# Kernel optimization log

Measured on AMD Instinct MI355X. Metric: run time of the kernel, lower is better.

The kernel has to match this reference:

```python
import jax, jax.numpy as jnp
import numpy as np

B, T, C, H = 4, 2048, 512, 8
HS = C // H  # head_size = 64
EPS = 1e-5


def layernorm(x, g, b):
    mu = jnp.mean(x, axis=-1, keepdims=True)
    var = jnp.mean(jnp.square(x - mu), axis=-1, keepdims=True)
    return (x - mu) * jax.lax.rsqrt(var + EPS) * g + b


def setup_inputs() -> dict:
    key = jax.random.key(0)
    ks = jax.random.split(key, 12)
    s_attn = 1.0 / np.sqrt(C)
    s_ff1 = 1.0 / np.sqrt(C)
    s_ff2 = 1.0 / np.sqrt(4 * C)
    return {
        "x": jax.random.normal(ks[0], (B, T, C), jnp.float32),
        "wq": jax.random.normal(ks[1], (H, C, HS), jnp.float32) * s_attn,
        "wk": jax.random.normal(ks[2], (H, C, HS), jnp.float32) * s_attn,
        "wv": jax.random.normal(ks[3], (H, C, HS), jnp.float32) * s_attn,
        "w1": jax.random.normal(ks[4], (C, 4 * C), jnp.float32) * s_ff1,
        "b1": jnp.zeros((4 * C,), jnp.float32),
        "w2": jax.random.normal(ks[5], (4 * C, C), jnp.float32) * s_ff2,
        "b2": jnp.zeros((C,), jnp.float32),
        "ln1_g": jnp.ones((C,), jnp.float32),
        "ln1_b": jnp.zeros((C,), jnp.float32),
        "ln2_g": jnp.ones((C,), jnp.float32),
        "ln2_b": jnp.zeros((C,), jnp.float32),
    }


def reference(x, wq, wk, wv, w1, b1, w2, b2, ln1_g, ln1_b, ln2_g, ln2_b):
    # pre-LN multi-head causal self-attention
    h = layernorm(x, ln1_g, ln1_b)                       # [B,T,C]
    q = jnp.einsum("btc,hcd->bhtd", h, wq)
    k = jnp.einsum("btc,hcd->bhtd", h, wk)
    v = jnp.einsum("btc,hcd->bhtd", h, wv)
    # NOTE: source scales by full embed dim C, not head_size
    scores = jnp.einsum("bhtd,bhsd->bhts", q, k) * (C ** -0.5)  # [B,H,T,T]
    causal = jnp.tril(jnp.ones((T, T), bool))
    scores = jnp.where(causal, scores, -jnp.inf)
    att = jax.nn.softmax(scores, axis=-1)
    out = jnp.einsum("bhts,bhsd->bhtd", att, v)          # [B,H,T,HS]
    out = out.transpose(0, 2, 1, 3).reshape(B, T, C)     # concat heads
    x = x + out
    # FFN with residual
    h2 = layernorm(x, ln2_g, ln2_b)
    ff = jax.nn.relu(h2 @ w1 + b1) @ w2 + b2
    return x + ff
```

## Files before the change

### kernel.cpp

```cpp
#include <hip/hip_runtime.h>

typedef unsigned short ushort_t;
typedef __attribute__((ext_vector_type(8))) short short8;
typedef __attribute__((ext_vector_type(4))) float floatx4;

#define B_  4
#define T_  2048
#define C_  512
#define H_  8
#define HS_ 64
#define M_  (B_*T_)
#define SCALE2 0.06376140168547404f

__device__ __forceinline__ float b2f(ushort_t u) {
  union { unsigned int i; float f; } w; w.i = ((unsigned int)u) << 16; return w.f;
}
__device__ __forceinline__ ushort_t f2b(float f) {
  union { float f; unsigned int i; } w; w.f = f;
  unsigned int x = w.i;
  return (ushort_t)((x + 0x7fffu + ((x >> 16) & 1u)) >> 16);
}
__device__ __forceinline__ ushort_t f2b_fast(float f) {
  union { float f; unsigned int i; } w; w.f = f;
  return (ushort_t)((w.i + 0x8000u) >> 16);
}
__device__ __forceinline__ void gl_lds16(const ushort_t* g, ushort_t* l) {
  __builtin_amdgcn_global_load_lds((const unsigned int*)g, (unsigned int*)l, 16, 0, 0);
}

__global__ __launch_bounds__(256) void transpose_all(const float* __restrict__ wq,
                                                     const float* __restrict__ wk,
                                                     const float* __restrict__ wv,
                                                     const float* __restrict__ w1,
                                                     const float* __restrict__ w2,
                                                     ushort_t* __restrict__ qkvt,
                                                     ushort_t* __restrict__ w1t,
                                                     ushort_t* __restrict__ w2t) {
  __shared__ ushort_t t[32][33];
  int idx = blockIdx.x;
  const float* in; ushort_t* out; int K, N, bx, by, z = 0;
  if (idx < 768) {
    int seg = idx >> 8, li = idx & 255;
    in = seg == 0 ? wq : (seg == 1 ? wk : wv);
    out = qkvt + (size_t)seg * 262144;
    K = 512; N = 64;
    z = li >> 5; li &= 31;
    bx = li & 1; by = li >> 1;
  } else if (idx < 1792) {
    int li = idx - 768;
    in = w1; out = w1t; K = 512; N = 2048;
    bx = li & 63; by = li >> 6;
  } else {
    int li = idx - 1792;
    in = w2; out = w2t; K = 2048; N = 512;
    bx = li & 15; by = li >> 4;
  }
  size_t zoff = (size_t)z * K * N;
  int n0 = bx * 32, k0 = by * 32;
  int tx = threadIdx.x & 31, ty = threadIdx.x >> 5;
#pragma unroll
  for (int i = 0; i < 4; i++)
    t[ty + 8 * i][tx] = f2b(in[zoff + (size_t)(k0 + ty + 8 * i) * N + n0 + tx]);
  __syncthreads();
#pragma unroll
  for (int i = 0; i < 4; i++)
    out[zoff + (size_t)(n0 + ty + 8 * i) * K + k0 + tx] = t[tx][ty + 8 * i];
}

__global__ __launch_bounds__(256) void ln_k(const float* __restrict__ X,
                                            const float* __restrict__ g,
                                            const float* __restrict__ bb,
                                            ushort_t* __restrict__ Y) {
  int wave = threadIdx.x >> 6, lane = threadIdx.x & 63;
  size_t row = (size_t)blockIdx.x * 4 + wave;
  float v[8], s = 0.f, s2 = 0.f;
#pragma unroll
  for (int i = 0; i < 8; i++) {
    float x = X[row * C_ + lane + 64 * i];
    v[i] = x; s += x; s2 += x * x;
  }
#pragma unroll
  for (int off = 32; off >= 1; off >>= 1) {
    s += __shfl_xor(s, off); s2 += __shfl_xor(s2, off);
  }
  float mu = s * (1.0f / C_);
  float var = s2 * (1.0f / C_) - mu * mu;
  float rs = rsqrtf(var + 1e-5f);
  ushort_t* yr = Y + row * C_;
#pragma unroll
  for (int i = 0; i < 8; i++) {
    int c = lane + 64 * i;
    yr[c] = f2b((v[i] - mu) * rs * g[c] + bb[c]);
  }
}

__global__ __launch_bounds__(256) void gemm_bt128(const ushort_t* __restrict__ A,
                                                  const ushort_t* __restrict__ Bt,
                                                  ushort_t* __restrict__ Out,
                                                  int K, int ldOut,
                                                  const float* __restrict__ bias,
                                                  int relu) {
  __shared__ __align__(16) ushort_t As[128 * 64];
  __shared__ __align__(16) ushort_t Bs[128 * 64];
  const int tid = threadIdx.x;
  const int lane = tid & 63, wave = tid >> 6;
  const long row0 = (long)blockIdx.x * 128;
  const long col0 = (long)blockIdx.y * 128;
  const int srow = wave * 32 + (lane >> 3);
  const int scol = (((lane & 7) ^ ((lane >> 3) & 7))) * 8;
  const ushort_t* Ab = A + (size_t)(row0 + srow) * K + scol;
  const ushort_t* Bb = Bt + (size_t)(col0 + srow) * K + scol;
  const int wm = (wave >> 1) * 64, wn = (wave & 1) * 64;
  const int fq = lane >> 4, fl = lane & 15;
  floatx4 acc[4][4] = {};

  for (int k0 = 0; k0 < K; k0 += 64) {
    __syncthreads();
#pragma unroll
    for (int i = 0; i < 4; i++) {
      gl_lds16(Ab + (size_t)(i * 8) * K + k0, &As[(wave * 32 + i * 8) * 64]);
      gl_lds16(Bb + (size_t)(i * 8) * K + k0, &Bs[(wave * 32 + i * 8) * 64]);
    }
    __syncthreads();
#pragma unroll
    for (int ks = 0; ks < 2; ks++) {
      short8 af[4], bf[4];
      const int sl = ((ks * 4 + fq) ^ (fl & 7)) * 8;
#pragma unroll
      for (int i = 0; i < 4; i++) {
        af[i] = *(const short8*)&As[(wm + i * 16 + fl) * 64 + sl];
        bf[i] = *(const short8*)&Bs[(wn + i * 16 + fl) * 64 + sl];
      }
#pragma unroll
      for (int fi = 0; fi < 4; fi++)
#pragma unroll
        for (int fj = 0; fj < 4; fj++)
          acc[fi][fj] = __builtin_amdgcn_mfma_f32_16x16x32_bf16(af[fi], bf[fj], acc[fi][fj], 0, 0, 0);
    }
  }
#pragma unroll
  for (int fi = 0; fi < 4; fi++)
#pragma unroll
    for (int fj = 0; fj < 4; fj++) {
      long gcol = col0 + wn + fj * 16 + fl;
      float bv = bias ? bias[gcol] : 0.0f;
#pragma unroll
      for (int r = 0; r < 4; r++) {
        long grow = row0 + wm + fi * 16 + fq * 4 + r;
        float v = acc[fi][fj][r] + bv;
        if (relu) v = fmaxf(v, 0.0f);
        Out[(size_t)grow * ldOut + gcol] = f2b(v);
      }
    }
}

__global__ __launch_bounds__(256) void gemm_bt64(const ushort_t* __restrict__ A,
                                                 const ushort_t* __restrict__ Bt,
                                                 float* __restrict__ Out,
                                                 int K, int ldOut,
                                                 const float* __restrict__ bias,
                                                 const float* __restrict__ residual) {
  __shared__ __align__(16) ushort_t As[64 * 64];
  __shared__ __align__(16) ushort_t Bs[64 * 64];
  const int tid = threadIdx.x;
  const int lane = tid & 63, wave = tid >> 6;
  const long row0 = (long)blockIdx.x * 64;
  const long col0 = (long)blockIdx.y * 64;
  const int srow = wave * 16 + (lane >> 3);
  const int scol = (((lane & 7) ^ ((lane >> 3) & 7))) * 8;
  const ushort_t* Ab = A + (size_t)(row0 + srow) * K + scol;
  const ushort_t* Bb = Bt + (size_t)(col0 + srow) * K + scol;
  const int wm = (wave >> 1) * 32, wn = (wave & 1) * 32;
  const int fq = lane >> 4, fl = lane & 15;
  floatx4 acc[2][2] = {};

  for (int k0 = 0; k0 < K; k0 += 64) {
    __syncthreads();
#pragma unroll
    for (int i = 0; i < 2; i++) {
      gl_lds16(Ab + (size_t)(i * 8) * K + k0, &As[(wave * 16 + i * 8) * 64]);
      gl_lds16(Bb + (size_t)(i * 8) * K + k0, &Bs[(wave * 16 + i * 8) * 64]);
    }
    __syncthreads();
#pragma unroll
    for (int ks = 0; ks < 2; ks++) {
      short8 af[2], bf[2];
      const int sl = ((ks * 4 + fq) ^ (fl & 7)) * 8;
#pragma unroll
      for (int i = 0; i < 2; i++) {
        af[i] = *(const short8*)&As[(wm + i * 16 + fl) * 64 + sl];
        bf[i] = *(const short8*)&Bs[(wn + i * 16 + fl) * 64 + sl];
      }
#pragma unroll
      for (int fi = 0; fi < 2; fi++)
#pragma unroll
        for (int fj = 0; fj < 2; fj++)
          acc[fi][fj] = __builtin_amdgcn_mfma_f32_16x16x32_bf16(af[fi], bf[fj], acc[fi][fj], 0, 0, 0);
    }
  }
#pragma unroll
  for (int fi = 0; fi < 2; fi++)
#pragma unroll
    for (int fj = 0; fj < 2; fj++) {
      long gcol = col0 + wn + fj * 16 + fl;
      float bv = bias[gcol];
#pragma unroll
      for (int r = 0; r < 4; r++) {
        long grow = row0 + wm + fi * 16 + fq * 4 + r;
        size_t oi = (size_t)grow * ldOut + gcol;
        Out[oi] = acc[fi][fj][r] + bv + residual[oi];
      }
    }
}

__global__ __launch_bounds__(512) void flash_attn(const ushort_t* __restrict__ QKV,
                                                  const float* __restrict__ X,
                                                  float* __restrict__ X1) {
  __shared__ __align__(16) ushort_t kt[64 * 72];
  __shared__ __align__(16) ushort_t vt[80 * 72];
  __shared__ __align__(16) ushort_t pt[128 * 72];
  const int tid = threadIdx.x;
  const int lane = tid & 63, wave = tid >> 6;
  const int fq = lane >> 4, fl = lane & 15;
  const int g = blockIdx.x >> 5;
  const int tile = g < 8 ? 15 - g : g - 8;
  const int bh = blockIdx.x & 31;
  const int h = bh & 7, b = bh >> 3;
  const int hoff = h * HS_;
  const int q0 = tile * 128;
  const int LD = 3 * C_;
  const int nst = 2 * tile + 2;
  const int whalf = wave >> 2;

  for (int i = tid; i < 16 * 72; i += 512) {
    int rr = i / 72;
    vt[(64 + rr) * 72 + (i % 72)] = (rr == 0) ? (ushort_t)0x3F80 : (ushort_t)0;
  }

  short8 qf0, qf1;
  {
    const ushort_t* qp = QKV + (size_t)((size_t)b * T_ + q0 + wave * 16 + fl) * LD + hoff + fq * 8;
    qf0 = *(const short8*)(qp);
    qf1 = *(const short8*)(qp + 32);
  }
  floatx4 oacc[4] = {};
  floatx4 lacc = {};

  const int role = tid >> 8;
  const int t2 = tid & 255;
  const int sr2 = (t2 >> 3) * 2;
  const int d0 = (t2 & 7) * 8;
  const ushort_t* sbase = QKV + (size_t)((size_t)b * T_ + sr2) * LD + hoff +
                          (role ? C_ : 2 * C_);

  short8 r0 = *(const short8*)(sbase + d0);
  short8 r1 = *(const short8*)(sbase + LD + d0);

  for (int st = 0; st < nst; st++) {
    __syncthreads();
    if (role) {
      *(short8*)&kt[sr2 * 72 + d0] = r0;
      *(short8*)&kt[(sr2 + 1) * 72 + d0] = r1;
    } else {
#pragma unroll
      for (int i = 0; i < 8; i++) {
        int d = d0 + i;
        int scol = sr2 ^ (8 * (d >> 3));
        unsigned int pk = ((unsigned int)(ushort_t)r0[i]) |
                          (((unsigned int)(ushort_t)r1[i]) << 16);
        *(unsigned int*)&vt[d * 72 + scol] = pk;
      }
    }
    __syncthreads();

    if (st < nst - 1) {
      const ushort_t* sp = sbase + (size_t)(st + 1) * 64 * LD;
      r0 = *(const short8*)(sp + d0);
      r1 = *(const short8*)(sp + LD + d0);
    }

    if (!(whalf == 0 && st == nst - 1)) {
      int s0 = st * 64;
      floatx4 sacc[4] = {};
#pragma unroll
      for (int fn = 0; fn < 4; fn++) {
        short8 kf0 = *(const short8*)&kt[(fn * 16 + fl) * 72 + fq * 8];
        short8 kf1 = *(const short8*)&kt[(fn * 16 + fl) * 72 + 32 + fq * 8];
        sacc[fn] = __builtin_amdgcn_mfma_f32_16x16x32_bf16(qf0, kf0, sacc[fn], 0, 0, 0);
        sacc[fn] = __builtin_amdgcn_mfma_f32_16x16x32_bf16(qf1, kf1, sacc[fn], 0, 0, 0);
      }
      bool diag = (st == 2 * tile + whalf);
#pragma unroll
      for (int fn = 0; fn < 4; fn++)
#pragma unroll
        for (int r = 0; r < 4; r++) {
          int qg = q0 + wave * 16 + fq * 4 + r;
          float p = exp2f(sacc[fn][r] * SCALE2);
          if (diag && (s0 + fn * 16 + fl) > qg) p = 0.0f;
          pt[(wave * 16 + fq * 4 + r) * 72 + fn * 16 + fl] = f2b_fast(p);
        }
      short8 pf0 = *(const short8*)&pt[(wave * 16 + fl) * 72 + fq * 8];
      short8 pf1 = *(const short8*)&pt[(wave * 16 + fl) * 72 + 32 + fq * 8];
#pragma unroll
      for (int fn = 0; fn < 4; fn++) {
        int drow = fn * 16 + fl;
        int sw = 8 * (drow >> 3);
        short8 vf0 = *(const short8*)&vt[drow * 72 + ((fq * 8) ^ sw)];
        short8 vf1 = *(const short8*)&vt[drow * 72 + ((32 + fq * 8) ^ sw)];
        oacc[fn] = __builtin_amdgcn_mfma_f32_16x16x32_bf16(pf0, vf0, oacc[fn], 0, 0, 0);
        oacc[fn] = __builtin_amdgcn_mfma_f32_16x16x32_bf16(pf1, vf1, oacc[fn], 0, 0, 0);
      }
      {
        short8 of0 = *(const short8*)&vt[(64 + fl) * 72 + fq * 8];
        short8 of1 = *(const short8*)&vt[(64 + fl) * 72 + 32 + fq * 8];
        lacc = __builtin_amdgcn_mfma_f32_16x16x32_bf16(pf0, of0, lacc, 0, 0, 0);
        lacc = __builtin_amdgcn_mfma_f32_16x16x32_bf16(pf1, of1, lacc, 0, 0, 0);
      }
    }
  }
#pragma unroll
  for (int r = 0; r < 4; r++) {
    float lr = __shfl(lacc[r], lane & 48);
    float inv = 1.0f / lr;
    int qg = q0 + wave * 16 + fq * 4 + r;
#pragma unroll
    for (int fn = 0; fn < 4; fn++) {
      int d = fn * 16 + fl;
      size_t oi = ((size_t)b * T_ + qg) * C_ + hoff + d;
      X1[oi] = oacc[fn][r] * inv + X[oi];
    }
  }
}

extern "C" void kernel_launch(void* const* d_in, const int* in_sizes, int n_in,
                              void* d_out, int out_size, void* d_ws, size_t ws_size,
                              hipStream_t stream) {
  const float* x  = (const float*)d_in[0];
  const float* wq = (const float*)d_in[1];
  const float* wk = (const float*)d_in[2];
  const float* wv = (const float*)d_in[3];
  const float* w1 = (const float*)d_in[4];
  const float* b1 = (const float*)d_in[5];
  const float* w2 = (const float*)d_in[6];
  const float* b2 = (const float*)d_in[7];
  const float* ln1g = (const float*)d_in[8];
  const float* ln1b = (const float*)d_in[9];
  const float* ln2g = (const float*)d_in[10];
  const float* ln2b = (const float*)d_in[11];
  ushort_t* ws = (ushort_t*)d_ws;

  const size_t SZ = (size_t)M_ * C_;
  ushort_t* qkvt = ws;
  ushort_t* w1t  = qkvt + 786432;
  ushort_t* w2t  = w1t + 1048576;
  ushort_t* qkv  = w2t + 1048576;
  ushort_t* h2   = qkv;
  ushort_t* ff1  = qkv + SZ;
  ushort_t* h    = (ushort_t*)d_out;
  float* x1      = (float*)d_out;
  float* outf    = (float*)d_out;

  transpose_all<<<2816, 256, 0, stream>>>(wq, wk, wv, w1, w2, qkvt, w1t, w2t);
  ln_k<<<M_ / 4, 256, 0, stream>>>(x, ln1g, ln1b, h);
  gemm_bt128<<<dim3(64, 12), 256, 0, stream>>>(h, qkvt, qkv, 512, 1536, nullptr, 0);
  flash_attn<<<B_ * H_ * (T_ / 128), 512, 0, stream>>>(qkv, x, x1);
  ln_k<<<M_ / 4, 256, 0, stream>>>(x1, ln2g, ln2b, h2);
  for (int p = 0; p < 2; p++) {
    const size_t roff = (size_t)p * 4096;
    gemm_bt128<<<dim3(32, 16), 256, 0, stream>>>(h2 + roff * C_, w1t, ff1,
                                                 512, 2048, b1, 1);
    gemm_bt64<<<dim3(64, 8), 256, 0, stream>>>(ff1, w2t, outf + roff * C_,
                                               2048, 512, b2, x1 + roff * C_);
  }
}
```

Measured before the change: 244.7 us.

## Double-buffer K/V in flash attention and pass P via register permutes

Double-buffers the K and V tiles in shared memory so each iteration needs one barrier instead of two, with the next tile's stores overlapping current compute. The score MFMA operands are swapped so each lane holds a column of the transposed scores. The probabilities are then packed with v_cvt_pk_bf16_f32 and redistributed with ds_bpermute instead of a round trip through an LDS P buffer. The softmax scale is folded into the Wq weights during the weight-prep transpose, and the ones-vector used for the row-sum MFMA now lives in registers. The cost is more LDS for the K/V buffers and extra permute instructions.

New measurement: 251.4 us. +2.7%, slower.

```diff
diff --git a/kernel.cpp b/kernel.cpp
--- a/kernel.cpp
+++ b/kernel.cpp
@@ -20,9 +20,10 @@
   unsigned int x = w.i;
   return (ushort_t)((x + 0x7fffu + ((x >> 16) & 1u)) >> 16);
 }
-__device__ __forceinline__ ushort_t f2b_fast(float f) {
-  union { float f; unsigned int i; } w; w.f = f;
-  return (ushort_t)((w.i + 0x8000u) >> 16);
+__device__ __forceinline__ unsigned int cvtpk(float a, float b) {
+  unsigned int r;
+  asm("v_cvt_pk_bf16_f32 %0, %1, %2" : "=v"(r) : "v"(a), "v"(b));
+  return r;
 }
 __device__ __forceinline__ void gl_lds16(const ushort_t* g, ushort_t* l) {
   __builtin_amdgcn_global_load_lds((const unsigned int*)g, (unsigned int*)l, 16, 0, 0);
@@ -39,6 +40,7 @@
   __shared__ ushort_t t[32][33];
   int idx = blockIdx.x;
   const float* in; ushort_t* out; int K, N, bx, by, z = 0;
+  float scl = (idx < 256) ? SCALE2 : 1.0f;
   if (idx < 768) {
     int seg = idx >> 8, li = idx & 255;
     in = seg == 0 ? wq : (seg == 1 ? wk : wv);
@@ -60,7 +62,7 @@
   int tx = threadIdx.x & 31, ty = threadIdx.x >> 5;
 #pragma unroll
   for (int i = 0; i < 4; i++)
-    t[ty + 8 * i][tx] = f2b(in[zoff + (size_t)(k0 + ty + 8 * i) * N + n0 + tx]);
+    t[ty + 8 * i][tx] = f2b(in[zoff + (size_t)(k0 + ty + 8 * i) * N + n0 + tx] * scl);
   __syncthreads();
 #pragma unroll
   for (int i = 0; i < 4; i++)
@@ -216,9 +218,8 @@
 __global__ __launch_bounds__(512) void flash_attn(const ushort_t* __restrict__ QKV,
                                                   const float* __restrict__ X,
                                                   float* __restrict__ X1) {
-  __shared__ __align__(16) ushort_t kt[64 * 72];
-  __shared__ __align__(16) ushort_t vt[80 * 72];
-  __shared__ __align__(16) ushort_t pt[128 * 72];
+  __shared__ __align__(16) ushort_t kt[2][64 * 72];
+  __shared__ __align__(16) ushort_t vt[2][64 * 72];
   const int tid = threadIdx.x;
   const int lane = tid & 63, wave = tid >> 6;
   const int fq = lane >> 4, fl = lane & 15;
@@ -231,17 +232,19 @@
   const int LD = 3 * C_;
   const int nst = 2 * tile + 2;
   const int whalf = wave >> 2;
-
-  for (int i = tid; i < 16 * 72; i += 512) {
-    int rr = i / 72;
-    vt[(64 + rr) * 72 + (i % 72)] = (rr == 0) ? (ushort_t)0x3F80 : (ushort_t)0;
-  }
+  const int qg = q0 + wave * 16 + fl;
 
   short8 qf0, qf1;
   {
     const ushort_t* qp = QKV + (size_t)((size_t)b * T_ + q0 + wave * 16 + fl) * LD + hoff + fq * 8;
     qf0 = *(const short8*)(qp);
     qf1 = *(const short8*)(qp + 32);
+  }
+  short8 of;
+  {
+    short ob = (fl == 0) ? (short)0x3F80 : (short)0;
+#pragma unroll
+    for (int i = 0; i < 8; i++) of[i] = ob;
   }
   floatx4 oacc[4] = {};
   floatx4 lacc = {};
@@ -253,80 +256,113 @@
   const ushort_t* sbase = QKV + (size_t)((size_t)b * T_ + sr2) * LD + hoff +
                           (role ? C_ : 2 * C_);
 
+  const int addrA = ((2 * (fq & 1)) * 16 + fl) * 4;
+  const int addrB = addrA + 64;
+  const bool lowq = fq < 2;
+
   short8 r0 = *(const short8*)(sbase + d0);
   short8 r1 = *(const short8*)(sbase + LD + d0);
+  if (role) {
+    *(short8*)&kt[0][sr2 * 72 + d0] = r0;
+    *(short8*)&kt[0][(sr2 + 1) * 72 + d0] = r1;
+  } else {
+#pragma unroll
+    for (int i = 0; i < 8; i++) {
+      int d = d0 + i;
+      int scol = sr2 ^ (8 * (d >> 3));
+      unsigned int pk = ((unsigned int)(ushort_t)r0[i]) |
+                        (((unsigned int)(ushort_t)r1[i]) << 16);
+      *(unsigned int*)&vt[0][d * 72 + scol] = pk;
+    }
+  }
+  {
+    const ushort_t* sp = sbase + (size_t)64 * LD;
+    r0 = *(const short8*)(sp + d0);
+    r1 = *(const short8*)(sp + LD + d0);
+  }
 
   for (int st = 0; st < nst; st++) {
     __syncthreads();
-    if (role) {
-      *(short8*)&kt[sr2 * 72 + d0] = r0;
-      *(short8*)&kt[(sr2 + 1) * 72 + d0] = r1;
-    } else {
-#pragma unroll
-      for (int i = 0; i < 8; i++) {
-        int d = d0 + i;
-        int scol = sr2 ^ (8 * (d >> 3));
-        unsigned int pk = ((unsigned int)(ushort_t)r0[i]) |
-                          (((unsigned int)(ushort_t)r1[i]) << 16);
-        *(unsigned int*)&vt[d * 72 + scol] = pk;
-      }
-    }
-    __syncthreads();
-
-    if (st < nst - 1) {
-      const ushort_t* sp = sbase + (size_t)(st + 1) * 64 * LD;
-      r0 = *(const short8*)(sp + d0);
-      r1 = *(const short8*)(sp + LD + d0);
+    const int cur = st & 1;
+    if (st + 1 < nst) {
+      const int nb = cur ^ 1;
+      if (role) {
+        *(short8*)&kt[nb][sr2 * 72 + d0] = r0;
+        *(short8*)&kt[nb][(sr2 + 1) * 72 + d0] = r1;
+      } else {
+#pragma unroll
+        for (int i = 0; i < 8; i++) {
+          int d = d0 + i;
+          int scol = sr2 ^ (8 * (d >> 3));
+          unsigned int pk = ((unsigned int)(ushort_t)r0[i]) |
+                            (((unsigned int)(ushort_t)r1[i]) << 16);
+          *(unsigned int*)&vt[nb][d * 72 + scol] = pk;
+        }
+      }
+      if (st + 2 < nst) {
+        const ushort_t* sp = sbase + (size_t)(st + 2) * 64 * LD;
+        r0 = *(const short8*)(sp + d0);
+        r1 = *(const short8*)(sp + LD + d0);
+      }
     }
 
     if (!(whalf == 0 && st == nst - 1)) {
-      int s0 = st * 64;
+      const int s0 = st * 64;
       floatx4 sacc[4] = {};
 #pragma unroll
       for (int fn = 0; fn < 4; fn++) {
-        short8 kf0 = *(const short8*)&kt[(fn * 16 + fl) * 72 + fq * 8];
-        short8 kf1 = *(const short8*)&kt[(fn * 16 + fl) * 72 + 32 + fq * 8];
-        sacc[fn] = __builtin_amdgcn_mfma_f32_16x16x32_bf16(qf0, kf0, sacc[fn], 0, 0, 0);
-        sacc[fn] = __builtin_amdgcn_mfma_f32_16x16x32_bf16(qf1, kf1, sacc[fn], 0, 0, 0);
-      }
-      bool diag = (st == 2 * tile + whalf);
-#pragma unroll
-      for (int fn = 0; fn < 4; fn++)
+        short8 kf0 = *(const short8*)&kt[cur][(fn * 16 + fl) * 72 + fq * 8];
+        short8 kf1 = *(const short8*)&kt[cur][(fn * 16 + fl) * 72 + 32 + fq * 8];
+        sacc[fn] = __builtin_amdgcn_mfma_f32_16x16x32_bf16(kf0, qf0, sacc[fn], 0, 0, 0);
+        sacc[fn] = __builtin_amdgcn_mfma_f32_16x16x32_bf16(kf1, qf1, sacc[fn], 0, 0, 0);
+      }
+      const bool diag = (st == 2 * tile + whalf);
+      unsigned int xc[4][2];
+#pragma unroll
+      for (int fn = 0; fn < 4; fn++) {
+        float p[4];
 #pragma unroll
         for (int r = 0; r < 4; r++) {
-          int qg = q0 + wave * 16 + fq * 4 + r;
-          float p = exp2f(sacc[fn][r] * SCALE2);
-          if (diag && (s0 + fn * 16 + fl) > qg) p = 0.0f;
-          pt[(wave * 16 + fq * 4 + r) * 72 + fn * 16 + fl] = f2b_fast(p);
+          float pv = exp2f(sacc[fn][r]);
+          if (diag && (s0 + fn * 16 + fq * 4 + r) > qg) pv = 0.0f;
+          p[r] = pv;
         }
-      short8 pf0 = *(const short8*)&pt[(wave * 16 + fl) * 72 + fq * 8];
-      short8 pf1 = *(const short8*)&pt[(wave * 16 + fl) * 72 + 32 + fq * 8];
+        xc[fn][0] = cvtpk(p[0], p[1]);
+        xc[fn][1] = cvtpk(p[2], p[3]);
+      }
+      union U8 { unsigned int u[4]; short8 s8; } pu[2];
+#pragma unroll
+      for (int o = 0; o < 2; o++)
+#pragma unroll
+        for (int t = 0; t < 4; t++) {
+          int ad = (t >> 1) ? addrB : addrA;
+          int lo = __builtin_amdgcn_ds_bpermute(ad, (int)xc[2 * o][t & 1]);
+          int hi = __builtin_amdgcn_ds_bpermute(ad, (int)xc[2 * o + 1][t & 1]);
+          pu[o].u[t] = lowq ? (unsigned int)lo : (unsigned int)hi;
+        }
+      short8 pf0 = pu[0].s8, pf1 = pu[1].s8;
 #pragma unroll
       for (int fn = 0; fn < 4; fn++) {
         int drow = fn * 16 + fl;
         int sw = 8 * (drow >> 3);
-        short8 vf0 = *(const short8*)&vt[drow * 72 + ((fq * 8) ^ sw)];
-        short8 vf1 = *(const short8*)&vt[drow * 72 + ((32 + fq * 8) ^ sw)];
+        short8 vf0 = *(const short8*)&vt[cur][drow * 72 + ((fq * 8) ^ sw)];
+        short8 vf1 = *(const short8*)&vt[cur][drow * 72 + ((32 + fq * 8) ^ sw)];
         oacc[fn] = __builtin_amdgcn_mfma_f32_16x16x32_bf16(pf0, vf0, oacc[fn], 0, 0, 0);
         oacc[fn] = __builtin_amdgcn_mfma_f32_16x16x32_bf16(pf1, vf1, oacc[fn], 0, 0, 0);
       }
-      {
-        short8 of0 = *(const short8*)&vt[(64 + fl) * 72 + fq * 8];
-        short8 of1 = *(const short8*)&vt[(64 + fl) * 72 + 32 + fq * 8];
-        lacc = __builtin_amdgcn_mfma_f32_16x16x32_bf16(pf0, of0, lacc, 0, 0, 0);
-        lacc = __builtin_amdgcn_mfma_f32_16x16x32_bf16(pf1, of1, lacc, 0, 0, 0);
-      }
+      lacc = __builtin_amdgcn_mfma_f32_16x16x32_bf16(pf0, of, lacc, 0, 0, 0);
+      lacc = __builtin_amdgcn_mfma_f32_16x16x32_bf16(pf1, of, lacc, 0, 0, 0);
     }
   }
 #pragma unroll
   for (int r = 0; r < 4; r++) {
     float lr = __shfl(lacc[r], lane & 48);
     float inv = 1.0f / lr;
-    int qg = q0 + wave * 16 + fq * 4 + r;
+    int qgr = q0 + wave * 16 + fq * 4 + r;
 #pragma unroll
     for (int fn = 0; fn < 4; fn++) {
       int d = fn * 16 + fl;
-      size_t oi = ((size_t)b * T_ + qg) * C_ + hoff + d;
+      size_t oi = ((size_t)b * T_ + qgr) * C_ + hoff + d;
       X1[oi] = oacc[fn][r] * inv + X[oi];
     }
   }
```
